# Kernel tuning notes

Measured on AMD Instinct MI355X. Metric: run time of the kernel, lower is better.

Reference implementation:

```python
import jax, jax.numpy as jnp
import numpy as np

B, N, R = 32768, 9, 4
IN_DIM = 5
DIMS = [64, 128, 256]
BN_EPS = 1e-5
LRELU_SLOPE = 0.2


def _rgcn_block(h, adj, ws, wr, b, gamma, beta):
    # Relational GCN: self transform + per-relation aggregation
    hw = jnp.einsum('bnd,rde->brne', h, wr)        # [B,R,N,D]
    agg = jnp.einsum('brmn,brne->bme', adj, hw)    # [B,N,D]
    h = h @ ws + agg + b
    # BatchNorm1d(max_num_atoms): channel axis is the atom index (training-mode batch stats)
    mean = jnp.mean(h, axis=(0, 2), keepdims=True)
    var = jnp.var(h, axis=(0, 2), keepdims=True)
    h = (h - mean) * jax.lax.rsqrt(var + BN_EPS)
    h = h * gamma[None, :, None] + beta[None, :, None]
    # LeakyReLU(0.2)
    return jnp.where(h > 0, h, LRELU_SLOPE * h)


def setup_inputs() -> dict:
    key = jax.random.key(0)
    ks = jax.random.split(key, 10)
    inp = {
        'atom_feats': jax.random.normal(ks[0], (B, N, IN_DIM), jnp.float32),
        'adj': jax.random.uniform(ks[1], (B, R, N, N), jnp.float32),
        'mask': jnp.ones((B, N), jnp.float32),
    }
    dims = [IN_DIM] + DIMS
    for i in range(3):
        din, dout = dims[i], dims[i + 1]
        inp[f'w_self{i}'] = jax.random.normal(ks[2 + 2 * i], (din, dout), jnp.float32) / np.sqrt(din)
        inp[f'w_rel{i}'] = jax.random.normal(ks[3 + 2 * i], (R, din, dout), jnp.float32) / np.sqrt(din)
        inp[f'b{i}'] = jnp.zeros((dout,), jnp.float32)
        inp[f'g{i}'] = jnp.ones((N,), jnp.float32)
        inp[f'be{i}'] = jnp.zeros((N,), jnp.float32)
    inp['fc_w'] = jax.random.normal(ks[8], (DIMS[-1], 1), jnp.float32) / np.sqrt(DIMS[-1])
    inp['fc_b'] = jnp.zeros((1,), jnp.float32)
    return inp


def reference(atom_feats, adj, mask,
              w_self0, w_rel0, b0, g0, be0,
              w_self1, w_rel1, b1, g1, be1,
              w_self2, w_rel2, b2, g2, be2,
              fc_w, fc_b):
    h = atom_feats
    h = _rgcn_block(h, adj, w_self0, w_rel0, b0, g0, be0)
    h = _rgcn_block(h, adj, w_self1, w_rel1, b1, g1, be1)
    h = _rgcn_block(h, adj, w_self2, w_rel2, b2, g2, be2)
    # masked sum readout
    g = jnp.sum(h * mask[:, :, None], axis=1)   # [B,D]
    out = g @ fc_w + fc_b                        # [B,1]
    return out.squeeze(-1)
```

## Files before the change

kernel.cpp:

```cpp
#include <hip/hip_runtime.h>
#include <hip/hip_bf16.h>


#define NB 32768
#define NA 9
#define NR 4
#define D0 5
#define D1 64
#define D2 128
#define D3 256
#define EPS 1e-5f
#define SLOPE 0.2f
#define NSLOT 64

typedef __hip_bfloat16 bf16;
typedef short bf16x8 __attribute__((ext_vector_type(8)));
typedef float f32x4 __attribute__((ext_vector_type(4)));

__device__ __forceinline__ float bf2f(bf16 v) { return __bfloat162float(v); }
__device__ __forceinline__ bf16  f2bf(float v) { return __float2bfloat16(v); }

__global__ __launch_bounds__(256) void k_zero(float* __restrict__ hdr, float* __restrict__ out)
{
    int idx = blockIdx.x * 256 + threadIdx.x;
    if (idx < NB) out[idx] = 0.f;
    if (idx < 6240) hdr[idx] = 0.f;
}

template<int DIN, int DOUT>
__global__ __launch_bounds__(256) void k_prep(const float* __restrict__ ws,
                                              const float* __restrict__ wr,
                                              bf16* __restrict__ wt)
{
    constexpr int K5 = 5*DIN;
    int idx = blockIdx.x*256 + threadIdx.x;
    if (idx >= DOUT*K5) return;
    int n = idx / K5, k = idx % K5;
    int s = k / DIN, kk = k % DIN;
    float v = (s == 0) ? ws[(size_t)kk*DOUT + n]
                       : wr[((size_t)(s-1)*DIN + kk)*DOUT + n];
    wt[idx] = f2bf(v);
}

__global__ __launch_bounds__(256) void k_layer0(
    const float* __restrict__ feats,
    const float* __restrict__ adj,
    const float* __restrict__ ws,
    const float* __restrict__ wr,
    const float* __restrict__ bias,
    bf16* __restrict__ hpre,
    float* __restrict__ slots)
{
    __shared__ float Wsh[5][5][64];
    __shared__ float Bsh[64];
    __shared__ float Adj[4][4][9][9];
    __shared__ float Hsh[4][9][5];
    __shared__ float bstat[18];

    int tid = threadIdx.x;
    int bl  = tid >> 6;
    int e   = tid & 63;
    int b0  = blockIdx.x * 4;

    for (int i = tid; i < 5*64; i += 256) Wsh[0][i/64][i%64] = ws[i];
    for (int i = tid; i < 4*5*64; i += 256) {
        int s = i / 320, rem = i % 320;
        Wsh[1+s][rem/64][rem%64] = wr[i];
    }
    if (tid < 64) Bsh[tid] = bias[tid];
    if (tid < 18) bstat[tid] = 0.f;
    {
        const float* ap = adj + (size_t)(b0 + bl) * (NR*NA*NA);
        float* dst = &Adj[bl][0][0][0];
        for (int i = e; i < NR*NA*NA; i += 64) dst[i] = ap[i];
    }
    {
        const float* fp = feats + (size_t)(b0 + bl) * (NA*D0);
        float* dst = &Hsh[bl][0][0];
        for (int i = e; i < NA*D0; i += 64) dst[i] = fp[i];
    }
    __syncthreads();

    float X[5][9];
    #pragma unroll
    for (int s = 0; s < 5; s++)
        #pragma unroll
        for (int n = 0; n < 9; n++) {
            float a = 0.f;
            #pragma unroll
            for (int k = 0; k < 5; k++) a += Hsh[bl][n][k] * Wsh[s][k][e];
            X[s][n] = a;
        }
    float bv = Bsh[e];
    float out[9];
    #pragma unroll
    for (int m = 0; m < 9; m++) {
        float a = X[0][m] + bv;
        #pragma unroll
        for (int r = 0; r < 4; r++)
            #pragma unroll
            for (int n = 0; n < 9; n++)
                a += Adj[bl][r][m][n] * X[1+r][n];
        out[m] = a;
    }
    bf16* hp = hpre + (size_t)(b0 + bl) * (NA*D1) + e;
    #pragma unroll
    for (int m = 0; m < 9; m++) hp[m*D1] = f2bf(out[m]);

    #pragma unroll
    for (int m = 0; m < 9; m++) {
        float s = out[m], q = out[m]*out[m];
        #pragma unroll
        for (int off = 32; off > 0; off >>= 1) {
            s += __shfl_xor(s, off, 64);
            q += __shfl_xor(q, off, 64);
        }
        if (e == 0) { atomicAdd(&bstat[m], s); atomicAdd(&bstat[9+m], q); }
    }
    __syncthreads();
    if (tid < 9) {
        float* sl = slots + (size_t)(blockIdx.x & (NSLOT-1)) * 32;
        atomicAdd(&sl[tid],      bstat[tid]);
        atomicAdd(&sl[16+tid],   bstat[9+tid]);
    }
}

template<int DOUT>
__global__ void k_finalize(const float* __restrict__ slots,
                           const float* __restrict__ g, const float* __restrict__ be,
                           float* __restrict__ fin)
{
    int n = threadIdx.x;
    if (n < 9) {
        float s = 0.f, q = 0.f;
        for (int i = 0; i < NSLOT; i++) { s += slots[i*32+n]; q += slots[i*32+16+n]; }
        float cnt = (float)NB * (float)DOUT;
        float mean = s / cnt;
        float var  = q / cnt - mean*mean;
        float sc   = g[n] * rsqrtf(var + EPS);
        fin[n]    = sc;
        fin[16+n] = be[n] - mean * sc;
    }
}

template<int DIN>
__device__ __forceinline__ void buildY(int j, int tid, int off,
    const bf16* hS, const float* adjS, bf16* ydst)
{
    constexpr int HS = DIN + 8;
    constexpr int KS = DIN/32;
    int r = j / KS, k0c = (j % KS)*32;
    #pragma unroll
    for (int ii = 0; ii < 2; ii++) {
        int i = tid + ii*256;
        int row_l = i >> 3;
        int c4 = (i & 7)*4;
        int loc = off + row_l;
        int ml = loc / 9;
        int a = loc - ml*9;
        const float* apj = adjS + ml*324 + r*81 + a*9;
        const bf16* hp = hS + (ml*9)*HS + k0c + c4;
        float f0=0.f, f1=0.f, f2=0.f, f3=0.f;
        #pragma unroll
        for (int n = 0; n < 9; n++) {
            float av = apj[n];
            bf16 hv[4] __attribute__((aligned(8)));
            *(uint2*)hv = *(const uint2*)(hp + n*HS);
            f0 += av*bf2f(hv[0]); f1 += av*bf2f(hv[1]);
            f2 += av*bf2f(hv[2]); f3 += av*bf2f(hv[3]);
        }
        bf16 ov[4] __attribute__((aligned(8)));
        ov[0]=f2bf(f0); ov[1]=f2bf(f1); ov[2]=f2bf(f2); ov[3]=f2bf(f3);
        *(uint2*)(ydst + row_l*40 + c4) = *(uint2*)ov;
    }
}

template<int DIN, int DOUT, int MODE>
__global__ __launch_bounds__(256, 3) void k_mfma(
    const bf16*  __restrict__ hprev,
    const float* __restrict__ finPrev,
    const float* __restrict__ adjg,
    const bf16*  __restrict__ wt,
    const float* __restrict__ bias,
    bf16*  __restrict__ hout,
    float* __restrict__ slots,
    const float* __restrict__ finC,
    const float* __restrict__ maskg,
    const float* __restrict__ fcw,
    float* __restrict__ outp)
{
    constexpr int K5 = 5*DIN;
    constexpr int HS = DIN + 8;
    constexpr int NT = DOUT/64;
    constexpr int KS = DIN/32;
    constexpr int NRS = 4*KS;

    __shared__ __align__(16) bf16 hS[81*HS];
    __shared__ __align__(16) bf16 yS[2*64*40];
    __shared__ float adjS[9*324];
    __shared__ float rstat[128];
    __shared__ float sfinP[32];
    __shared__ float sfinC[32];

    int tid = threadIdx.x;
    int row0 = blockIdx.x * 64;
    int mol_lo = row0 / 9;
    int mol_hi = (row0 + 63) / 9;
    int nmol = mol_hi - mol_lo + 1;
    int off = row0 - mol_lo*9;

    if (tid < 32) sfinP[tid] = finPrev[tid];
    if constexpr (MODE == 2) { if (tid >= 32 && tid < 64) sfinC[tid-32] = finC[tid-32]; }
    if (tid >= 64 && tid < 192) rstat[tid-64] = 0.f;
    for (int i = tid; i < nmol*324; i += 256) adjS[i] = adjg[(size_t)mol_lo*324 + i];
    __syncthreads();

    constexpr int HW4 = DIN/4;
    for (int i = tid; i < nmol*9*HW4; i += 256) {
        int rl = i / HW4;
        int a  = rl % 9;
        int c4 = (i % HW4)*4;
        bf16 hv[4] __attribute__((aligned(8)));
        *(uint2*)hv = *(const uint2*)(hprev + (size_t)(mol_lo*9 + rl)*DIN + c4);
        float sc = sfinP[a], sh = sfinP[16+a];
        bf16 ov[4] __attribute__((aligned(8)));
        #pragma unroll
        for (int jj = 0; jj < 4; jj++) {
            float v = sc*bf2f(hv[jj]) + sh;
            v = v > 0.f ? v : SLOPE*v;
            ov[jj] = f2bf(v);
        }
        *(uint2*)(&hS[rl*HS + c4]) = *(uint2*)ov;
    }
    __syncthreads();

    int wv = tid >> 6, lane = tid & 63;
    int q = lane >> 4, l15 = lane & 15;

    f32x4 acc[4][NT];
    #pragma unroll
    for (int mt = 0; mt < 4; mt++)
        #pragma unroll
        for (int t = 0; t < NT; t++) acc[mt][t] = (f32x4){0.f, 0.f, 0.f, 0.f};

    const bf16* wp[NT];
    #pragma unroll
    for (int t = 0; t < NT; t++) {
        int ncol = (wv*NT + t)*16 + l15;
        wp[t] = wt + (size_t)ncol*K5 + q*8;
    }

    #pragma unroll
    for (int ks = 0; ks < KS; ks++) {
        bf16x8 Af[4], Bf[NT];
        #pragma unroll
        for (int mt = 0; mt < 4; mt++)
            Af[mt] = *(const bf16x8*)(hS + (size_t)(off + mt*16 + l15)*HS + ks*32 + q*8);
        #pragma unroll
        for (int t = 0; t < NT; t++)
            Bf[t] = *(const bf16x8*)(wp[t] + ks*32);
        #pragma unroll
        for (int mt = 0; mt < 4; mt++)
            #pragma unroll
            for (int t = 0; t < NT; t++)
                acc[mt][t] = __builtin_amdgcn_mfma_f32_16x16x32_bf16(Af[mt], Bf[t], acc[mt][t], 0, 0, 0);
    }

    buildY<DIN>(0, tid, off, hS, adjS, yS);
    __syncthreads();
    for (int j = 0; j < NRS; j++) {
        int kc = KS + j;
        const bf16* yb = yS + (size_t)(j & 1)*(64*40);
        bf16x8 Af[4], Bf[NT];
        #pragma unroll
        for (int mt = 0; mt < 4; mt++)
            Af[mt] = *(const bf16x8*)(yb + (size_t)(mt*16 + l15)*40 + q*8);
        #pragma unroll
        for (int t = 0; t < NT; t++)
            Bf[t] = *(const bf16x8*)(wp[t] + kc*32);
        #pragma unroll
        for (int mt = 0; mt < 4; mt++)
            #pragma unroll
            for (int t = 0; t < NT; t++)
                acc[mt][t] = __builtin_amdgcn_mfma_f32_16x16x32_bf16(Af[mt], Bf[t], acc[mt][t], 0, 0, 0);
        if (j + 1 < NRS)
            buildY<DIN>(j + 1, tid, off, hS, adjS, yS + (size_t)((j + 1) & 1)*(64*40));
        __syncthreads();
    }

    float bcol[NT];
    #pragma unroll
    for (int t = 0; t < NT; t++) bcol[t] = bias[(wv*NT + t)*16 + l15];

    if constexpr (MODE == 2) {
        float fwv[NT];
        #pragma unroll
        for (int t = 0; t < NT; t++) fwv[t] = fcw[(wv*NT + t)*16 + l15];
        #pragma unroll
        for (int mt = 0; mt < 4; mt++) {
            #pragma unroll
            for (int reg = 0; reg < 4; reg++) {
                int rloc = mt*16 + q*4 + reg;
                int atom = (row0 + rloc) % 9;
                float sc = sfinC[atom], sh = sfinC[16+atom];
                float part = 0.f;
                #pragma unroll
                for (int t = 0; t < NT; t++) {
                    float v = acc[mt][t][reg] + bcol[t];
                    float y = sc*v + sh;
                    y = y > 0.f ? y : SLOPE*y;
                    part += y * fwv[t];
                }
                part += __shfl_xor(part, 1); part += __shfl_xor(part, 2);
                part += __shfl_xor(part, 4); part += __shfl_xor(part, 8);
                if (l15 == 0) atomicAdd(&rstat[rloc], part);
            }
        }
        __syncthreads();
        if (tid < 64) {
            int rg = row0 + tid;
            int b = rg / 9;
            atomicAdd(&outp[b], rstat[tid] * maskg[rg]);
        }
        return;
    }

    #pragma unroll
    for (int mt = 0; mt < 4; mt++) {
        #pragma unroll
        for (int reg = 0; reg < 4; reg++) {
            int rloc = mt*16 + q*4 + reg;
            float s = 0.f, qq = 0.f;
            #pragma unroll
            for (int t = 0; t < NT; t++) {
                float v = acc[mt][t][reg] + bcol[t];
                if constexpr (MODE == 0) {
                    size_t o = (size_t)(row0 + rloc)*DOUT + (wv*NT + t)*16 + l15;
                    hout[o] = f2bf(v);
                }
                s += v; qq += v*v;
            }
            s += __shfl_xor(s, 1); s += __shfl_xor(s, 2);
            s += __shfl_xor(s, 4); s += __shfl_xor(s, 8);
            qq += __shfl_xor(qq, 1); qq += __shfl_xor(qq, 2);
            qq += __shfl_xor(qq, 4); qq += __shfl_xor(qq, 8);
            if (l15 == 0) { atomicAdd(&rstat[rloc*2], s); atomicAdd(&rstat[rloc*2+1], qq); }
        }
    }
    __syncthreads();
    if (tid < 64) {
        int rg = row0 + tid;
        int atom = rg % 9;
        float* sl = slots + (size_t)(blockIdx.x & (NSLOT-1))*32;
        atomicAdd(&sl[atom],    rstat[tid*2]);
        atomicAdd(&sl[16+atom], rstat[tid*2+1]);
    }
}

__global__ __launch_bounds__(256) void k_readout(
    const bf16* __restrict__ h2,
    const float* __restrict__ fin,
    const float* __restrict__ mask,
    const float* __restrict__ fcw,
    const float* __restrict__ fcb,
    float* __restrict__ out)
{
    int tid = threadIdx.x;
    int w = tid >> 6, lane = tid & 63;
    int b = blockIdx.x * 4 + w;
    float sc[9], sh[9];
    #pragma unroll
    for (int n = 0; n < 9; n++) { sc[n] = fin[n]; sh[n] = fin[16+n]; }
    const bf16* hp = h2 + (size_t)b * (NA*D3) + lane*4;
    float acc0 = 0.f, acc1 = 0.f, acc2 = 0.f, acc3 = 0.f;
    #pragma unroll
    for (int n = 0; n < 9; n++) {
        bf16 v4[4] __attribute__((aligned(8)));
        *(uint2*)v4 = *(const uint2*)(hp + n*D3);
        float mk = mask[(size_t)b*NA + n];
        float v;
        v = sc[n]*bf2f(v4[0]) + sh[n]; v = v > 0.f ? v : SLOPE*v; acc0 += v*mk;
        v = sc[n]*bf2f(v4[1]) + sh[n]; v = v > 0.f ? v : SLOPE*v; acc1 += v*mk;
        v = sc[n]*bf2f(v4[2]) + sh[n]; v = v > 0.f ? v : SLOPE*v; acc2 += v*mk;
        v = sc[n]*bf2f(v4[3]) + sh[n]; v = v > 0.f ? v : SLOPE*v; acc3 += v*mk;
    }
    float4 wv = *(const float4*)(fcw + lane*4);
    float s = acc0*wv.x + acc1*wv.y + acc2*wv.z + acc3*wv.w;
    #pragma unroll
    for (int off = 1; off < 64; off <<= 1) s += __shfl_xor(s, off, 64);
    if (lane == 0) out[b] = s + fcb[0];
}

__global__ __launch_bounds__(256) void k_addfcb(float* __restrict__ out, const float* __restrict__ fcb)
{
    int idx = blockIdx.x * 256 + threadIdx.x;
    if (idx < NB) out[idx] += fcb[0];
}


extern "C" void kernel_launch(void* const* d_in, const int* in_sizes, int n_in,
                              void* d_out, int out_size, void* d_ws, size_t ws_size,
                              hipStream_t stream)
{
    const float* feats = (const float*)d_in[0];
    const float* adj   = (const float*)d_in[1];
    const float* mask  = (const float*)d_in[2];
    const float* ws0 = (const float*)d_in[3];
    const float* wr0 = (const float*)d_in[4];
    const float* b0  = (const float*)d_in[5];
    const float* g0  = (const float*)d_in[6];
    const float* be0 = (const float*)d_in[7];
    const float* ws1 = (const float*)d_in[8];
    const float* wr1 = (const float*)d_in[9];
    const float* b1  = (const float*)d_in[10];
    const float* g1  = (const float*)d_in[11];
    const float* be1 = (const float*)d_in[12];
    const float* ws2 = (const float*)d_in[13];
    const float* wr2 = (const float*)d_in[14];
    const float* b2  = (const float*)d_in[15];
    const float* g2  = (const float*)d_in[16];
    const float* be2 = (const float*)d_in[17];
    const float* fcw = (const float*)d_in[18];
    const float* fcb = (const float*)d_in[19];
    float* outp = (float*)d_out;

    char* wsb = (char*)d_ws;
    float* slots0 = (float*)(wsb + 0);
    float* slots1 = slots0 + NSLOT*32;
    float* slots2 = slots1 + NSLOT*32;
    float* fin0 = (float*)(wsb + 24576);
    float* fin1 = fin0 + 32;
    float* fin2 = fin1 + 32;
    bf16* wt1 = (bf16*)(wsb + 32768);
    bf16* wt2 = (bf16*)(wsb + 114688);

    k_zero<<<(NB+255)/256, 256, 0, stream>>>((float*)wsb, outp);
    k_prep<D1, D2><<<(D2*5*D1 + 255)/256, 256, 0, stream>>>(ws1, wr1, wt1);
    k_prep<D2, D3><<<(D3*5*D2 + 255)/256, 256, 0, stream>>>(ws2, wr2, wt2);

    bool bigws = (ws_size >= 227016704ULL);
    const int GRID = (NB*NA)/64;

    if (bigws) {
        bf16* h1 = (bf16*)(wsb + 524288ULL);
        bf16* h2 = (bf16*)(wsb + 76021760ULL);
        bf16* h0 = h2;

        k_layer0<<<NB/4, 256, 0, stream>>>(feats, adj, ws0, wr0, b0, h0, slots0);
        k_finalize<D1><<<1, 64, 0, stream>>>(slots0, g0, be0, fin0);

        k_mfma<D1, D2, 0><<<GRID, 256, 0, stream>>>(
            h0, fin0, adj, wt1, b1, h1, slots1, nullptr, nullptr, nullptr, nullptr);
        k_finalize<D2><<<1, 64, 0, stream>>>(slots1, g1, be1, fin1);

        k_mfma<D2, D3, 0><<<GRID, 256, 0, stream>>>(
            h1, fin1, adj, wt2, b2, h2, slots2, nullptr, nullptr, nullptr, nullptr);
        k_finalize<D3><<<1, 64, 0, stream>>>(slots2, g2, be2, fin2);

        k_readout<<<NB/4, 256, 0, stream>>>(h2, fin2, mask, fcw, fcb, outp);
    } else {
        bf16* h0 = (bf16*)(wsb + 524288ULL);
        bf16* h1 = (bf16*)(wsb + 38273024ULL);

        k_layer0<<<NB/4, 256, 0, stream>>>(feats, adj, ws0, wr0, b0, h0, slots0);
        k_finalize<D1><<<1, 64, 0, stream>>>(slots0, g0, be0, fin0);

        k_mfma<D1, D2, 0><<<GRID, 256, 0, stream>>>(
            h0, fin0, adj, wt1, b1, h1, slots1, nullptr, nullptr, nullptr, nullptr);
        k_finalize<D2><<<1, 64, 0, stream>>>(slots1, g1, be1, fin1);

        k_mfma<D2, D3, 1><<<GRID, 256, 0, stream>>>(
            h1, fin1, adj, wt2, b2, nullptr, slots2, nullptr, nullptr, nullptr, nullptr);
        k_finalize<D3><<<1, 64, 0, stream>>>(slots2, g2, be2, fin2);

        k_mfma<D2, D3, 2><<<GRID, 256, 0, stream>>>(
            h1, fin1, adj, wt2, b2, nullptr, nullptr, fin2, mask, fcw, outp);
        k_addfcb<<<(NB+255)/256, 256, 0, stream>>>(outp, fcb);
    }
}
```

Before: 627.4 us.

## Register-cache adjacency and compute all relations per K-chunk with packed FMA

Each thread now loads its row's adjacency coefficients for all four relations into registers instead of staging all molecules' adjacency in shared memory. The relation-aggregation build computes all four relation outputs for a 32-column chunk at once using packed f32x2 FMAs, reusing each loaded h row across relations. It then runs the MFMAs for those four relations, replacing the double-buffered per-relation pipeline. Staging loads are widened to 8 bf16 values, and LeakyReLU uses fmaxf. This is meant to cut LDS traffic and redundant h reads, at the cost of more registers (36 adjacency floats plus 32 accumulators) and a larger yS buffer, which may lower occupancy.

```diff
diff --git a/kernel.cpp b/kernel.cpp
--- a/kernel.cpp
+++ b/kernel.cpp
@@ -12,13 +12,35 @@
 #define EPS 1e-5f
 #define SLOPE 0.2f
 #define NSLOT 64
+#define YST 56
 
 typedef __hip_bfloat16 bf16;
 typedef short bf16x8 __attribute__((ext_vector_type(8)));
 typedef float f32x4 __attribute__((ext_vector_type(4)));
+typedef float f32x2 __attribute__((ext_vector_type(2)));
 
 __device__ __forceinline__ float bf2f(bf16 v) { return __bfloat162float(v); }
 __device__ __forceinline__ bf16  f2bf(float v) { return __float2bfloat16(v); }
+
+__device__ __forceinline__ void cvt8(bf16x8 v, f32x2 out[4]) {
+    union { bf16x8 h; unsigned u[4]; } cv; cv.h = v;
+    #pragma unroll
+    for (int j = 0; j < 4; j++) {
+        out[j].x = __uint_as_float(cv.u[j] << 16);
+        out[j].y = __uint_as_float(cv.u[j] & 0xffff0000u);
+    }
+}
+
+__device__ __forceinline__ bf16x8 pack8(const f32x2 y[4]) {
+    union { bf16x8 h; unsigned short s[8]; } cv;
+    #pragma unroll
+    for (int j = 0; j < 4; j++) {
+        union { bf16 b; unsigned short s; } t0, t1;
+        t0.b = f2bf(y[j].x); t1.b = f2bf(y[j].y);
+        cv.s[2*j] = t0.s; cv.s[2*j+1] = t1.s;
+    }
+    return cv.h;
+}
 
 __global__ __launch_bounds__(256) void k_zero(float* __restrict__ hdr, float* __restrict__ out)
 {
@@ -43,13 +65,9 @@
 }
 
 __global__ __launch_bounds__(256) void k_layer0(
-    const float* __restrict__ feats,
-    const float* __restrict__ adj,
-    const float* __restrict__ ws,
-    const float* __restrict__ wr,
-    const float* __restrict__ bias,
-    bf16* __restrict__ hpre,
-    float* __restrict__ slots)
+    const float* __restrict__ feats, const float* __restrict__ adj,
+    const float* __restrict__ ws, const float* __restrict__ wr,
+    const float* __restrict__ bias, bf16* __restrict__ hpre, float* __restrict__ slots)
 {
     __shared__ float Wsh[5][5][64];
     __shared__ float Bsh[64];
@@ -140,38 +158,6 @@
         float sc   = g[n] * rsqrtf(var + EPS);
         fin[n]    = sc;
         fin[16+n] = be[n] - mean * sc;
-    }
-}
-
-template<int DIN>
-__device__ __forceinline__ void buildY(int j, int tid, int off,
-    const bf16* hS, const float* adjS, bf16* ydst)
-{
-    constexpr int HS = DIN + 8;
-    constexpr int KS = DIN/32;
-    int r = j / KS, k0c = (j % KS)*32;
-    #pragma unroll
-    for (int ii = 0; ii < 2; ii++) {
-        int i = tid + ii*256;
-        int row_l = i >> 3;
-        int c4 = (i & 7)*4;
-        int loc = off + row_l;
-        int ml = loc / 9;
-        int a = loc - ml*9;
-        const float* apj = adjS + ml*324 + r*81 + a*9;
-        const bf16* hp = hS + (ml*9)*HS + k0c + c4;
-        float f0=0.f, f1=0.f, f2=0.f, f3=0.f;
-        #pragma unroll
-        for (int n = 0; n < 9; n++) {
-            float av = apj[n];
-            bf16 hv[4] __attribute__((aligned(8)));
-            *(uint2*)hv = *(const uint2*)(hp + n*HS);
-            f0 += av*bf2f(hv[0]); f1 += av*bf2f(hv[1]);
-            f2 += av*bf2f(hv[2]); f3 += av*bf2f(hv[3]);
-        }
-        bf16 ov[4] __attribute__((aligned(8)));
-        ov[0]=f2bf(f0); ov[1]=f2bf(f1); ov[2]=f2bf(f2); ov[3]=f2bf(f3);
-        *(uint2*)(ydst + row_l*40 + c4) = *(uint2*)ov;
     }
 }
 
@@ -193,11 +179,10 @@
     constexpr int HS = DIN + 8;
     constexpr int NT = DOUT/64;
     constexpr int KS = DIN/32;
-    constexpr int NRS = 4*KS;
+    constexpr int HW8 = DIN/8;
 
     __shared__ __align__(16) bf16 hS[81*HS];
-    __shared__ __align__(16) bf16 yS[2*64*40];
-    __shared__ float adjS[9*324];
+    __shared__ __align__(16) bf16 yS[4*64*YST];
     __shared__ float rstat[128];
     __shared__ float sfinP[32];
     __shared__ float sfinC[32];
@@ -212,25 +197,37 @@
     if (tid < 32) sfinP[tid] = finPrev[tid];
     if constexpr (MODE == 2) { if (tid >= 32 && tid < 64) sfinC[tid-32] = finC[tid-32]; }
     if (tid >= 64 && tid < 192) rstat[tid-64] = 0.f;
-    for (int i = tid; i < nmol*324; i += 256) adjS[i] = adjg[(size_t)mol_lo*324 + i];
+
+    int brow = tid >> 2;
+    int bc8  = (tid & 3) * 8;
+    int bloc = off + brow;
+    int bml  = bloc / 9;
+    int ba   = bloc - bml*9;
+    float adjR[4][9];
+    {
+        const float* ap = adjg + (size_t)(mol_lo + bml)*324 + ba*9;
+        #pragma unroll
+        for (int r = 0; r < 4; r++)
+            #pragma unroll
+            for (int n = 0; n < 9; n++) adjR[r][n] = ap[r*81 + n];
+    }
     __syncthreads();
 
-    constexpr int HW4 = DIN/4;
-    for (int i = tid; i < nmol*9*HW4; i += 256) {
-        int rl = i / HW4;
+    for (int i = tid; i < nmol*9*HW8; i += 256) {
+        int rl = i / HW8;
         int a  = rl % 9;
-        int c4 = (i % HW4)*4;
-        bf16 hv[4] __attribute__((aligned(8)));
-        *(uint2*)hv = *(const uint2*)(hprev + (size_t)(mol_lo*9 + rl)*DIN + c4);
+        int c8 = (i % HW8)*8;
+        bf16x8 hv = *(const bf16x8*)(hprev + (size_t)(mol_lo*9 + rl)*DIN + c8);
+        f32x2 hf[4]; cvt8(hv, hf);
         float sc = sfinP[a], sh = sfinP[16+a];
-        bf16 ov[4] __attribute__((aligned(8)));
-        #pragma unroll
-        for (int jj = 0; jj < 4; jj++) {
-            float v = sc*bf2f(hv[jj]) + sh;
-            v = v > 0.f ? v : SLOPE*v;
-            ov[jj] = f2bf(v);
-        }
-        *(uint2*)(&hS[rl*HS + c4]) = *(uint2*)ov;
+        f32x2 o[4];
+        #pragma unroll
+        for (int j = 0; j < 4; j++) {
+            float v0 = sc*hf[j].x + sh; v0 = fmaxf(v0, SLOPE*v0);
+            float v1 = sc*hf[j].y + sh; v1 = fmaxf(v1, SLOPE*v1);
+            o[j] = (f32x2){v0, v1};
+        }
+        *(bf16x8*)(&hS[rl*HS + c8]) = pack8(o);
     }
     __syncthreads();
 
@@ -245,10 +242,8 @@
 
     const bf16* wp[NT];
     #pragma unroll
-    for (int t = 0; t < NT; t++) {
-        int ncol = (wv*NT + t)*16 + l15;
-        wp[t] = wt + (size_t)ncol*K5 + q*8;
-    }
+    for (int t = 0; t < NT; t++)
+        wp[t] = wt + (size_t)((wv*NT + t)*16 + l15)*K5 + q*8;
 
     #pragma unroll
     for (int ks = 0; ks < KS; ks++) {
@@ -266,25 +261,47 @@
                 acc[mt][t] = __builtin_amdgcn_mfma_f32_16x16x32_bf16(Af[mt], Bf[t], acc[mt][t], 0, 0, 0);
     }
 
-    buildY<DIN>(0, tid, off, hS, adjS, yS);
-    __syncthreads();
-    for (int j = 0; j < NRS; j++) {
-        int kc = KS + j;
-        const bf16* yb = yS + (size_t)(j & 1)*(64*40);
-        bf16x8 Af[4], Bf[NT];
-        #pragma unroll
-        for (int mt = 0; mt < 4; mt++)
-            Af[mt] = *(const bf16x8*)(yb + (size_t)(mt*16 + l15)*40 + q*8);
-        #pragma unroll
-        for (int t = 0; t < NT; t++)
-            Bf[t] = *(const bf16x8*)(wp[t] + kc*32);
-        #pragma unroll
-        for (int mt = 0; mt < 4; mt++)
+    for (int kc = 0; kc < KS; kc++) {
+        {
+            const bf16* hb = hS + (size_t)(bml*9)*HS + kc*32 + bc8;
+            f32x2 y[4][4];
+            #pragma unroll
+            for (int r = 0; r < 4; r++)
+                #pragma unroll
+                for (int j = 0; j < 4; j++) y[r][j] = (f32x2){0.f, 0.f};
+            #pragma unroll
+            for (int n = 0; n < 9; n++) {
+                bf16x8 hv = *(const bf16x8*)(hb + n*HS);
+                f32x2 hf[4]; cvt8(hv, hf);
+                #pragma unroll
+                for (int r = 0; r < 4; r++) {
+                    f32x2 av = (f32x2){adjR[r][n], adjR[r][n]};
+                    #pragma unroll
+                    for (int j = 0; j < 4; j++)
+                        y[r][j] = __builtin_elementwise_fma(av, hf[j], y[r][j]);
+                }
+            }
+            #pragma unroll
+            for (int r = 0; r < 4; r++)
+                *(bf16x8*)(&yS[(r*64 + brow)*YST + bc8]) = pack8(y[r]);
+        }
+        __syncthreads();
+        #pragma unroll
+        for (int r = 0; r < 4; r++) {
+            int kcol = DIN + (r*KS + kc)*32;
+            bf16x8 Af[4], Bf[NT];
+            #pragma unroll
+            for (int mt = 0; mt < 4; mt++)
+                Af[mt] = *(const bf16x8*)(&yS[(r*64 + mt*16 + l15)*YST + q*8]);
             #pragma unroll
             for (int t = 0; t < NT; t++)
-                acc[mt][t] = __builtin_amdgcn_mfma_f32_16x16x32_bf16(Af[mt], Bf[t], acc[mt][t], 0, 0, 0);
-        if (j + 1 < NRS)
-            buildY<DIN>(j + 1, tid, off, hS, adjS, yS + (size_t)((j + 1) & 1)*(64*40));
+                Bf[t] = *(const bf16x8*)(wp[t] + kcol);
+            #pragma unroll
+            for (int mt = 0; mt < 4; mt++)
+                #pragma unroll
+                for (int t = 0; t < NT; t++)
+                    acc[mt][t] = __builtin_amdgcn_mfma_f32_16x16x32_bf16(Af[mt], Bf[t], acc[mt][t], 0, 0, 0);
+        }
         __syncthreads();
     }
 
@@ -308,7 +325,7 @@
                 for (int t = 0; t < NT; t++) {
                     float v = acc[mt][t][reg] + bcol[t];
                     float y = sc*v + sh;
-                    y = y > 0.f ? y : SLOPE*y;
+                    y = fmaxf(y, SLOPE*y);
                     part += y * fwv[t];
                 }
                 part += __shfl_xor(part, 1); part += __shfl_xor(part, 2);
@@ -358,12 +375,9 @@
 }
 
 __global__ __launch_bounds__(256) void k_readout(
-    const bf16* __restrict__ h2,
-    const float* __restrict__ fin,
-    const float* __restrict__ mask,
-    const float* __restrict__ fcw,
-    const float* __restrict__ fcb,
-    float* __restrict__ out)
+    const bf16* __restrict__ h2, const float* __restrict__ fin,
+    const float* __restrict__ mask, const float* __restrict__ fcw,
+    const float* __restrict__ fcb, float* __restrict__ out)
 {
     int tid = threadIdx.x;
     int w = tid >> 6, lane = tid & 63;
@@ -379,10 +393,10 @@
         *(uint2*)v4 = *(const uint2*)(hp + n*D3);
         float mk = mask[(size_t)b*NA + n];
         float v;
-        v = sc[n]*bf2f(v4[0]) + sh[n]; v = v > 0.f ? v : SLOPE*v; acc0 += v*mk;
-        v = sc[n]*bf2f(v4[1]) + sh[n]; v = v > 0.f ? v : SLOPE*v; acc1 += v*mk;
-        v = sc[n]*bf2f(v4[2]) + sh[n]; v = v > 0.f ? v : SLOPE*v; acc2 += v*mk;
-        v = sc[n]*bf2f(v4[3]) + sh[n]; v = v > 0.f ? v : SLOPE*v; acc3 += v*mk;
+        v = sc[n]*bf2f(v4[0]) + sh[n]; v = fmaxf(v, SLOPE*v); acc0 += v*mk;
+        v = sc[n]*bf2f(v4[1]) + sh[n]; v = fmaxf(v, SLOPE*v); acc1 += v*mk;
+        v = sc[n]*bf2f(v4[2]) + sh[n]; v = fmaxf(v, SLOPE*v); acc2 += v*mk;
+        v = sc[n]*bf2f(v4[3]) + sh[n]; v = fmaxf(v, SLOPE*v); acc3 += v*mk;
     }
     float4 wv = *(const float4*)(fcw + lane*4);
     float s = acc0*wv.x + acc1*wv.y + acc2*wv.z + acc3*wv.w;
```

Result: slower. 704.4 us (+12.3%).
